# Performance work log

Hardware: AMD Instinct MI355X
Metric: run time of the kernel (lower is better)

## Reference

```python
import jax, jax.numpy as jnp
import numpy as np

B, N, S, DG, C_IN, C_OUT, HID = 2, 128, 4, 8, 4, 8, 32


def setup_inputs() -> dict:
    key = jax.random.key(0)
    ks = jax.random.split(key, 10)

    def w(k, shape, fan_in):
        return jax.random.normal(k, shape, jnp.float32) / np.float32(np.sqrt(fan_in))

    return {
        "pairwise_g": jax.random.normal(ks[0], (B, N, N, S, S, DG), jnp.float32),
        "coset_functions": jax.random.normal(ks[1], (B, N, S, C_IN), jnp.float32),
        "mask": jax.random.bernoulli(ks[2], 0.9, (B, N, S)),
        "ky_W1": w(ks[3], (C_IN, HID, 2), 2), "ky_b1": jnp.zeros((C_IN, HID), jnp.float32),
        "ky_W2": w(ks[4], (C_IN, HID, HID), HID), "ky_b2": jnp.zeros((C_IN, HID), jnp.float32),
        "ky_W3": w(ks[5], (C_IN, 1, HID), HID), "ky_b3": jnp.zeros((C_IN, 1), jnp.float32),
        "kg_W1": w(ks[6], (C_IN, HID, DG), DG), "kg_b1": jnp.zeros((C_IN, HID), jnp.float32),
        "kg_W2": w(ks[7], (C_IN, HID, HID), HID), "kg_b2": jnp.zeros((C_IN, HID), jnp.float32),
        "kg_W3": w(ks[8], (C_IN, 1, HID), HID), "kg_b3": jnp.zeros((C_IN, 1), jnp.float32),
        "w_out": w(ks[9], (C_OUT, C_IN), C_IN),
    }


def _mlp(x, W1, b1, W2, b2, W3, b3):
    # NerualNetKernel with bn=False, act=Swish: (Linear + SiLU) x 3, incl. output layer.
    h = jax.nn.silu(x @ W1.T + b1)
    h = jax.nn.silu(h @ W2.T + b2)
    return jax.nn.silu(h @ W3.T + b3)


def reference(pairwise_g, coset_functions, mask,
              ky_W1, ky_b1, ky_W2, ky_b2, ky_W3, ky_b3,
              kg_W1, kg_b1, kg_W2, kg_b2, kg_W3, kg_b3, w_out):
    b, n, _, s, _, _ = pairwise_g.shape
    c_in = coset_functions.shape[-1]
    key_mask = mask[:, None, :, None, :, None]  # (B,1,N,1,S,1) masks key points/samples
    outs = []
    for i in range(c_in):  # fixed small channel loop, as in the original module
        f = coset_functions[..., i:i + 1]  # (B,N,S,1)
        y1 = jnp.broadcast_to(f[:, None, :, None, :, :], (b, n, n, s, s, 1))  # key side
        y2 = jnp.broadcast_to(f[:, :, None, :, None, :], (b, n, n, s, s, 1))  # query side
        y = jnp.concatenate([y1, y2], axis=-1)  # (B,N,N,S,S,2)
        k = (_mlp(y, ky_W1[i], ky_b1[i], ky_W2[i], ky_b2[i], ky_W3[i], ky_b3[i])
             + _mlp(pairwise_g, kg_W1[i], kg_b1[i], kg_W2[i], kg_b2[i], kg_W3[i], kg_b3[i]))
        att = jnp.where(key_mask, jnp.exp(k), jnp.zeros((), k.dtype))  # (B,N,N,S,S,1)
        att = att / att.sum(axis=(2, 4), keepdims=True)
        f = f + (att * f[:, None, :, None, :, :]).sum(axis=(2, 4))  # residual + weighted agg
        outs.append(f)
    cf = jnp.concatenate(outs, axis=-1)  # (B,N,S,C_IN)
    cf = cf * mask[..., None].astype(cf.dtype)
    return cf @ w_out.T  # (B,N,S,C_OUT), bias-free output transform
```

## Files before the change

kernel.cpp:

```cpp
#include <hip/hip_runtime.h>
#include <hip/hip_bf16.h>

#define BB   2
#define NN   128
#define SS   4
#define DGG  8
#define CIN  4
#define COUT 8
#define HH   32
#define NT   512

typedef __attribute__((ext_vector_type(4))) float          fvec4;
typedef __attribute__((ext_vector_type(4))) unsigned short usvec4;
typedef __attribute__((ext_vector_type(8))) unsigned short usvec8;
typedef __attribute__((ext_vector_type(2))) __fp16         half2v;
typedef __attribute__((ext_vector_type(8))) __fp16         f16x8;
typedef __attribute__((ext_vector_type(4))) float          f32x4;
typedef __attribute__((ext_vector_type(4))) unsigned int   uvec4;

__device__ __forceinline__ float bf2f(unsigned short u) {
    return __uint_as_float(((unsigned int)u) << 16);
}
__device__ __forceinline__ float silu_f(float x) {
    float e = __builtin_amdgcn_exp2f(x * -1.44269504f);
    return x * __builtin_amdgcn_rcpf(1.0f + e);
}
__device__ __forceinline__ float exp_f(float x) {
    return __builtin_amdgcn_exp2f(x * 1.44269504f);
}

__device__ __forceinline__ unsigned int pk2u(float a, float b) {
#if __has_builtin(__builtin_amdgcn_cvt_pkrtz)
    half2v h = __builtin_amdgcn_cvt_pkrtz(a, b);
#else
    half2v h; h[0] = (__fp16)a; h[1] = (__fp16)b;
#endif
    union { half2v h; unsigned int u; } x; x.h = h; return x.u;
}
union FU { uvec4 u; f16x8 h; };
__device__ __forceinline__ f16x8 mk_frag(unsigned a, unsigned b, unsigned c, unsigned d) {
    FU x; x.u = (uvec4){a, b, c, d}; return x.h;
}
__device__ __forceinline__ f16x8 mk_fragv(uvec4 u) {
    FU x; x.u = u; return x.h;
}
__device__ __forceinline__ uvec4 vldu(const unsigned* p) {
    return *(volatile const uvec4*)p;
}
__device__ __forceinline__ fvec4 vldf(const float* p) {
    return *(volatile const fvec4*)p;
}
__device__ __forceinline__ f16x8 silu_frag(f32x4 a, f32x4 b) {
    return mk_frag(pk2u(silu_f(a[0]), silu_f(a[1])),
                   pk2u(silu_f(a[2]), silu_f(a[3])),
                   pk2u(silu_f(b[0]), silu_f(b[1])),
                   pk2u(silu_f(b[2]), silu_f(b[3])));
}

__device__ __forceinline__ float loadS(const void* p, int idx, int fmode) {
    return fmode ? bf2f(((const unsigned short*)p)[idx])
                 : ((const float*)p)[idx];
}
__device__ __forceinline__ void load8(const void* p, int base, int fmode, float* dst) {
    if (fmode) {
        usvec8 v = *(const usvec8*)((const unsigned short*)p + base);
#pragma unroll
        for (int d = 0; d < 8; ++d) dst[d] = bf2f(v[d]);
    } else {
        fvec4 a = *(const fvec4*)((const float*)p + base);
        fvec4 b = *(const fvec4*)((const float*)p + base + 4);
        dst[0] = a[0]; dst[1] = a[1]; dst[2] = a[2]; dst[3] = a[3];
        dst[4] = b[0]; dst[5] = b[1]; dst[6] = b[2]; dst[7] = b[3];
    }
}
__device__ __forceinline__ int load_mask(const void* p, int idx, int mmode) {
    if (mmode == 0) return ((const int*)p)[idx] != 0;
    if (mmode == 1) return ((const unsigned short*)p)[idx] != 0;
    if (mmode == 2) return ((const unsigned char*)p)[idx] != 0;
    return ((const unsigned int*)p)[idx] != 0;
}
__device__ __forceinline__ void stage_pk(unsigned int* dst, const void* src,
                                         int pairs, int fmode, int tid) {
    if (fmode) {
        const unsigned short* s = (const unsigned short*)src;
        for (int x = tid; x < pairs; x += NT)
            dst[x] = pk2u(bf2f(s[2 * x]), bf2f(s[2 * x + 1]));
    } else {
        const float* s = (const float*)src;
        for (int x = tid; x < pairs; x += NT)
            dst[x] = pk2u(s[2 * x], s[2 * x + 1]);
    }
}
__device__ __forceinline__ void copy_arr(float* sm, const void* src, int off,
                                         int cnt, int fmode, int tid) {
    if (fmode) {
        const unsigned short* s = (const unsigned short*)src;
        for (int x = tid; x < cnt; x += NT) sm[off + x] = bf2f(s[x]);
    } else {
        const float* s = (const float*)src;
        for (int x = tid; x < cnt; x += NT) sm[off + x] = s[x];
    }
}
__device__ __forceinline__ void detect_inline(const void* g_mask, const void* g_coset,
                                              int tid, int* smi, int slot) {
    if (tid < 64) {
        const unsigned short* cu = (const unsigned short*)g_coset;
        unsigned short v = cu[2 * tid];
        int e = (v >> 7) & 0xFF;
        int hits = __popcll(__ballot(e >= 110 && e <= 135));
        int fmode_ = (hits > 32) ? 1 : 0;
        const unsigned short* mu = (const unsigned short*)g_mask;
        int evenBF = 0, any3 = 0, anyByte = 0;
        for (int r = 0; r < 8; ++r) {
            int idx = tid + r * 64;
            unsigned short m = mu[idx];
            if (m == 0x3F80) { any3 = 1; if (!(idx & 1)) evenBF = 1; }
            if (m == 0x0101 || m == 0x0100) anyByte = 1;
        }
        evenBF  = (__ballot(evenBF)  != 0ull);
        any3    = (__ballot(any3)    != 0ull);
        anyByte = (__ballot(anyByte) != 0ull);
        if (tid == 0) {
            smi[slot]     = fmode_;
            smi[slot + 1] = evenBF ? 1 : (any3 ? 3 : (anyByte ? 2 : 0));
        }
    }
}

#define UG_G    0
#define F_FA    2048
#define U_YW1n  4096
#define U_GW1   4608
#define U_GB1q  5120
#define U_W2Y   5632
#define U_W2G   7680
#define F_YB2   9728
#define F_GB2   9856
#define U_YW3   9984
#define U_GW3   10048
#define F_YB3   10112
#define F_GB3   10116
#define U_CB1   10120
#define F_RED   10128
#define F_MODE  10192
#define U_TOTAL 10194

__global__ __launch_bounds__(NT, 8) void emha_mfma(
    const void* __restrict__ g_pw, const void* __restrict__ g_coset,
    const void* __restrict__ g_mask,
    const void* yW1, const void* yb1, const void* yW2, const void* yb2,
    const void* yW3, const void* yb3,
    const void* gW1, const void* gb1, const void* gW2, const void* gb2,
    const void* gW3, const void* gb3,
    const void* wout, void* outp)
{
    __shared__ __align__(16) unsigned int smu[U_TOTAL];
    float* smf = (float*)smu;
    int*   smi = (int*)smu;
    const int tid = threadIdx.x;

    detect_inline(g_mask, g_coset, tid, smi, F_MODE);
    __syncthreads();
    const int fmode = smi[F_MODE];
    const int mmode = smi[F_MODE + 1];
    __syncthreads();

    const int bn = blockIdx.x >> 2;
    const int s1 = blockIdx.x & 3;
    const int b  = bn >> 7;
    const int n1 = bn & 127;

    {
        const int pos = tid;
        const int n2 = pos >> 2, s2 = pos & 3;
        float g8[8];
        load8(g_pw, (((bn * NN + n2) * SS + s1) * SS + s2) * DGG, fmode, g8);
#pragma unroll
        for (int q = 0; q < 4; ++q)
            smu[UG_G + pos * 4 + q] = pk2u(g8[2 * q], g8[2 * q + 1]);
    }
    for (int x = tid; x < 2048; x += NT)
        smf[F_FA + x] = loadS(g_coset, b * 2048 + x, fmode);
    for (int x = tid; x < 128; x += NT) {
        smu[U_YW1n + x * 4 + 0] = pk2u(loadS(yW1, 2 * x, fmode), loadS(yW1, 2 * x + 1, fmode));
        smu[U_YW1n + x * 4 + 1] = pk2u(loadS(yb1, x, fmode), 0.f);
        smu[U_YW1n + x * 4 + 2] = 0u;
        smu[U_YW1n + x * 4 + 3] = 0u;
        smu[U_GB1q + x * 4 + 0] = pk2u(loadS(gb1, x, fmode), 0.f);
        smu[U_GB1q + x * 4 + 1] = 0u;
        smu[U_GB1q + x * 4 + 2] = 0u;
        smu[U_GB1q + x * 4 + 3] = 0u;
    }
    stage_pk(&smu[U_GW1], gW1, 512,  fmode, tid);
    stage_pk(&smu[U_W2Y], yW2, 2048, fmode, tid);
    stage_pk(&smu[U_W2G], gW2, 2048, fmode, tid);
    stage_pk(&smu[U_YW3], yW3, 64,   fmode, tid);
    stage_pk(&smu[U_GW3], gW3, 64,   fmode, tid);
    copy_arr(smf, yb2, F_YB2, 128, fmode, tid);
    copy_arr(smf, gb2, F_GB2, 128, fmode, tid);
    copy_arr(smf, yb3, F_YB3, 4, fmode, tid);
    copy_arr(smf, gb3, F_GB3, 4, fmode, tid);
    if (tid < 8) smu[U_CB1 + tid] = (tid == 0) ? 0x00003C00u : 0u;
    __syncthreads();

    const int lane = tid & 63;
    const int wave = tid >> 6;
    const int quad = lane >> 4;
    const int col  = lane & 15;
    const int qpos = n1 * 4 + s1;
    const int h0   = ((col >> 2) << 3) + (col & 3);

    const int mymask = load_mask(g_mask, b * 512 + wave * 64 + lane, mmode);
    const unsigned long long km64 = __ballot(mymask != 0);

    const unsigned* Zp = &smu[U_CB1 + 4];
    const f32x4 zf = {0.f, 0.f, 0.f, 0.f};

#pragma unroll 1
    for (int ci = 0; ci < CIN; ++ci) {
        const int rowy = (ci * 32 + h0) * 4;
        const unsigned* pAY1a = (quad == 0) ? &smu[U_YW1n + rowy] : Zp;
        const unsigned* pAY1b = (quad == 0) ? &smu[U_YW1n + rowy + 16] : Zp;
        const unsigned* pGA = (quad == 0) ? &smu[U_GW1 + rowy]
                            : ((quad == 1) ? &smu[U_GB1q + rowy] : Zp);
        const unsigned* pGB = (quad == 0) ? &smu[U_GW1 + rowy + 16]
                            : ((quad == 1) ? &smu[U_GB1q + rowy + 16] : Zp);
        const unsigned* pW2 = &smu[U_W2Y + ci * 512 + h0 * 16 + quad * 4];
        const float*    pCb = &smf[F_YB2 + ci * 32 + quad * 8];
        const unsigned* pA3y = (col == 0) ? &smu[U_YW3 + ci * 16 + quad * 4] : Zp;
        const unsigned* pA3g = (col == 0) ? &smu[U_GW3 + ci * 16 + quad * 4] : Zp;
        const unsigned* pBg = (quad == 0) ? &smu[UG_G + (wave * 64 + col) * 4]
                            : ((quad == 1) ? &smu[U_CB1] : Zp);
        const int stepBg = (quad == 0) ? 64 : 0;
        const float* pFA = &smf[F_FA + (wave * 64 + col) * 4 + ci];

        const float fb  = smf[F_FA + qpos * 4 + ci];
        const float b3y = smf[F_YB3 + ci];
        const float b3g = smf[F_GB3 + ci];

        float aN = 0.f, aD = 0.f;
        int amt = col;
#pragma unroll 1
        for (int t = 0; t < 4; ++t) {
            const uvec4 gq = vldu(pBg);
            const float fap = *(volatile const float*)pFA;
            const f16x8 Bg1 = mk_fragv(gq);
            const f16x8 B1y = mk_frag(pk2u(fap, fb), 0x00003C00u, 0u, 0u);

            f32x4 d1a, d1b, dga, dgb;
            {
                const f16x8 AY1a = mk_fragv(vldu(pAY1a));
                const f16x8 AY1b = mk_fragv(vldu(pAY1b));
                const f16x8 GA   = mk_fragv(vldu(pGA));
                const f16x8 GB   = mk_fragv(vldu(pGB));
#if defined(__HIP_DEVICE_COMPILE__)
                d1a = __builtin_amdgcn_mfma_f32_16x16x32_f16(AY1a, B1y, zf, 0, 0, 0);
                d1b = __builtin_amdgcn_mfma_f32_16x16x32_f16(AY1b, B1y, zf, 0, 0, 0);
                dga = __builtin_amdgcn_mfma_f32_16x16x32_f16(GA,   Bg1, zf, 0, 0, 0);
                dgb = __builtin_amdgcn_mfma_f32_16x16x32_f16(GB,   Bg1, zf, 0, 0, 0);
#else
                d1a = zf; d1b = zf; dga = zf; dgb = zf;
#endif
            }
            const f16x8 By = silu_frag(d1a, d1b);
            const f16x8 Bg = silu_frag(dga, dgb);

            f32x4 dy0, dy1, dg0, dg1;
            {
#if defined(__HIP_DEVICE_COMPILE__)
                dy0 = __builtin_amdgcn_mfma_f32_16x16x32_f16(mk_fragv(vldu(pW2)),        By, vldf(pCb),       0, 0, 0);
                dy1 = __builtin_amdgcn_mfma_f32_16x16x32_f16(mk_fragv(vldu(pW2 + 64)),   By, vldf(pCb + 4),   0, 0, 0);
                dg0 = __builtin_amdgcn_mfma_f32_16x16x32_f16(mk_fragv(vldu(pW2 + 2048)), Bg, vldf(pCb + 128), 0, 0, 0);
                dg1 = __builtin_amdgcn_mfma_f32_16x16x32_f16(mk_fragv(vldu(pW2 + 2112)), Bg, vldf(pCb + 132), 0, 0, 0);
#else
                dy0 = zf; dy1 = zf; dg0 = zf; dg1 = zf;
#endif
            }
            const f16x8 By2 = silu_frag(dy0, dy1);
            const f16x8 Bg2 = silu_frag(dg0, dg1);

            f32x4 dy3, dg3;
#if defined(__HIP_DEVICE_COMPILE__)
            dy3 = __builtin_amdgcn_mfma_f32_16x16x32_f16(mk_fragv(vldu(pA3y)), By2, zf, 0, 0, 0);
            dg3 = __builtin_amdgcn_mfma_f32_16x16x32_f16(mk_fragv(vldu(pA3g)), Bg2, zf, 0, 0, 0);
#else
            dy3 = zf; dg3 = zf;
#endif
            const float kyv = silu_f(dy3[0] + b3y);
            const float kgv = silu_f(dg3[0] + b3g);
            const int   kb  = (int)((km64 >> amt) & 1ull);
            const float e = kb ? exp_f(kyv + kgv) : 0.f;
            aD += e;
            aN += e * fap;

            amt += 16;
            pBg += stepBg;
            pFA += 64;
        }
        aN += __shfl_xor(aN, 1);  aD += __shfl_xor(aD, 1);
        aN += __shfl_xor(aN, 2);  aD += __shfl_xor(aD, 2);
        aN += __shfl_xor(aN, 4);  aD += __shfl_xor(aD, 4);
        aN += __shfl_xor(aN, 8);  aD += __shfl_xor(aD, 8);
        if (lane == 0) {
            smf[F_RED + (wave * 4 + ci) * 2 + 0] = aN;
            smf[F_RED + (wave * 4 + ci) * 2 + 1] = aD;
        }
    }
    __syncthreads();

    if (tid < COUT) {
        const int o = tid;
        const int m1 = load_mask(g_mask, b * 512 + qpos, mmode);
        float acc = 0.f;
#pragma unroll
        for (int ci = 0; ci < CIN; ++ci) {
            float N = 0.f, D = 0.f;
#pragma unroll
            for (int w = 0; w < 8; ++w) {
                N += smf[F_RED + (w * 4 + ci) * 2 + 0];
                D += smf[F_RED + (w * 4 + ci) * 2 + 1];
            }
            const float fbv = smf[F_FA + qpos * 4 + ci];
            const float cf = m1 ? (fbv + N / D) : 0.f;
            acc += cf * loadS(wout, o * CIN + ci, fmode);
        }
        const int oidx = (bn * SS + s1) * COUT + o;
        if (fmode) ((__hip_bfloat16*)outp)[oidx] = __float2bfloat16(acc);
        else       ((float*)outp)[oidx] = acc;
    }
}

extern "C" void kernel_launch(void* const* d_in, const int* in_sizes, int n_in,
                              void* d_out, int out_size, void* d_ws, size_t ws_size,
                              hipStream_t stream) {
    emha_mfma<<<BB * NN * SS, NT, 0, stream>>>(
        d_in[0], d_in[1], d_in[2],
        d_in[3], d_in[4], d_in[5], d_in[6], d_in[7], d_in[8],
        d_in[9], d_in[10], d_in[11], d_in[12], d_in[13], d_in[14],
        d_in[15], d_out);
}
```

Baseline: 197.7 us.

## Halve block size, hoist weight fragments into registers, drop volatile loads

Cuts threads per block from 512 to 256, so each wave now handles 128 key positions in 8 iterations instead of 64 in 4. The per-channel MLP weight and bias fragments are loaded from shared memory once, before the inner loop, rather than through volatile loads on every iteration. The mask ballot is split into two 64-bit masks, and the first barrier is merged so that mask loading overlaps staging. This trades more registers and fewer waves per block for less LDS traffic and more instruction-level parallelism.

New measurement: 168.9 us. 1.17x faster.

```diff
diff --git a/kernel.cpp b/kernel.cpp
--- a/kernel.cpp
+++ b/kernel.cpp
@@ -8,7 +8,7 @@
 #define CIN  4
 #define COUT 8
 #define HH   32
-#define NT   512
+#define NT   256
 
 typedef __attribute__((ext_vector_type(4))) float          fvec4;
 typedef __attribute__((ext_vector_type(4))) unsigned short usvec4;
@@ -43,12 +43,6 @@
 }
 __device__ __forceinline__ f16x8 mk_fragv(uvec4 u) {
     FU x; x.u = u; return x.h;
-}
-__device__ __forceinline__ uvec4 vldu(const unsigned* p) {
-    return *(volatile const uvec4*)p;
-}
-__device__ __forceinline__ fvec4 vldf(const float* p) {
-    return *(volatile const fvec4*)p;
 }
 __device__ __forceinline__ f16x8 silu_frag(f32x4 a, f32x4 b) {
     return mk_frag(pk2u(silu_f(a[0]), silu_f(a[1])),
@@ -142,10 +136,10 @@
 #define F_GB3   10116
 #define U_CB1   10120
 #define F_RED   10128
-#define F_MODE  10192
-#define U_TOTAL 10194
-
-__global__ __launch_bounds__(NT, 8) void emha_mfma(
+#define F_MODE  10160
+#define U_TOTAL 10162
+
+__global__ __launch_bounds__(NT, 4) void emha_mfma(
     const void* __restrict__ g_pw, const void* __restrict__ g_coset,
     const void* __restrict__ g_mask,
     const void* yW1, const void* yb1, const void* yW2, const void* yb2,
@@ -170,8 +164,9 @@
     const int b  = bn >> 7;
     const int n1 = bn & 127;
 
-    {
-        const int pos = tid;
+#pragma unroll
+    for (int it = 0; it < 2; ++it) {
+        const int pos = tid + it * 256;
         const int n2 = pos >> 2, s2 = pos & 3;
         float g8[8];
         load8(g_pw, (((bn * NN + n2) * SS + s1) * SS + s2) * DGG, fmode, g8);
@@ -201,99 +196,96 @@
     copy_arr(smf, yb3, F_YB3, 4, fmode, tid);
     copy_arr(smf, gb3, F_GB3, 4, fmode, tid);
     if (tid < 8) smu[U_CB1 + tid] = (tid == 0) ? 0x00003C00u : 0u;
-    __syncthreads();
 
     const int lane = tid & 63;
     const int wave = tid >> 6;
+    const int mLo = load_mask(g_mask, b * 512 + wave * 128 + lane, mmode);
+    const int mHi = load_mask(g_mask, b * 512 + wave * 128 + 64 + lane, mmode);
+    const unsigned long long kmL = __ballot(mLo != 0);
+    const unsigned long long kmH = __ballot(mHi != 0);
+    __syncthreads();
+
     const int quad = lane >> 4;
     const int col  = lane & 15;
     const int qpos = n1 * 4 + s1;
     const int h0   = ((col >> 2) << 3) + (col & 3);
-
-    const int mymask = load_mask(g_mask, b * 512 + wave * 64 + lane, mmode);
-    const unsigned long long km64 = __ballot(mymask != 0);
-
     const unsigned* Zp = &smu[U_CB1 + 4];
     const f32x4 zf = {0.f, 0.f, 0.f, 0.f};
 
 #pragma unroll 1
     for (int ci = 0; ci < CIN; ++ci) {
         const int rowy = (ci * 32 + h0) * 4;
-        const unsigned* pAY1a = (quad == 0) ? &smu[U_YW1n + rowy] : Zp;
-        const unsigned* pAY1b = (quad == 0) ? &smu[U_YW1n + rowy + 16] : Zp;
-        const unsigned* pGA = (quad == 0) ? &smu[U_GW1 + rowy]
-                            : ((quad == 1) ? &smu[U_GB1q + rowy] : Zp);
-        const unsigned* pGB = (quad == 0) ? &smu[U_GW1 + rowy + 16]
-                            : ((quad == 1) ? &smu[U_GB1q + rowy + 16] : Zp);
-        const unsigned* pW2 = &smu[U_W2Y + ci * 512 + h0 * 16 + quad * 4];
-        const float*    pCb = &smf[F_YB2 + ci * 32 + quad * 8];
-        const unsigned* pA3y = (col == 0) ? &smu[U_YW3 + ci * 16 + quad * 4] : Zp;
-        const unsigned* pA3g = (col == 0) ? &smu[U_GW3 + ci * 16 + quad * 4] : Zp;
-        const unsigned* pBg = (quad == 0) ? &smu[UG_G + (wave * 64 + col) * 4]
-                            : ((quad == 1) ? &smu[U_CB1] : Zp);
-        const int stepBg = (quad == 0) ? 64 : 0;
-        const float* pFA = &smf[F_FA + (wave * 64 + col) * 4 + ci];
+        const f16x8 AY1a = mk_fragv(*(const uvec4*)((quad == 0) ? &smu[U_YW1n + rowy] : Zp));
+        const f16x8 AY1b = mk_fragv(*(const uvec4*)((quad == 0) ? &smu[U_YW1n + rowy + 16] : Zp));
+        const f16x8 GA = mk_fragv(*(const uvec4*)((quad == 0) ? &smu[U_GW1 + rowy]
+                                   : (quad == 1) ? &smu[U_GB1q + rowy] : Zp));
+        const f16x8 GB = mk_fragv(*(const uvec4*)((quad == 0) ? &smu[U_GW1 + rowy + 16]
+                                   : (quad == 1) ? &smu[U_GB1q + rowy + 16] : Zp));
+        const f16x8 Ay0 = mk_fragv(*(const uvec4*)&smu[U_W2Y + ci * 512 + h0 * 16 + quad * 4]);
+        const f16x8 Ay1 = mk_fragv(*(const uvec4*)&smu[U_W2Y + ci * 512 + (h0 + 4) * 16 + quad * 4]);
+        const f16x8 Ag0 = mk_fragv(*(const uvec4*)&smu[U_W2G + ci * 512 + h0 * 16 + quad * 4]);
+        const f16x8 Ag1 = mk_fragv(*(const uvec4*)&smu[U_W2G + ci * 512 + (h0 + 4) * 16 + quad * 4]);
+        const fvec4 cY0 = *(const fvec4*)&smf[F_YB2 + ci * 32 + quad * 8];
+        const fvec4 cY1 = *(const fvec4*)&smf[F_YB2 + ci * 32 + quad * 8 + 4];
+        const fvec4 cG0 = *(const fvec4*)&smf[F_GB2 + ci * 32 + quad * 8];
+        const fvec4 cG1 = *(const fvec4*)&smf[F_GB2 + ci * 32 + quad * 8 + 4];
+        const f16x8 A3y = mk_fragv(*(const uvec4*)((col == 0) ? &smu[U_YW3 + ci * 16 + quad * 4] : Zp));
+        const f16x8 A3g = mk_fragv(*(const uvec4*)((col == 0) ? &smu[U_GW3 + ci * 16 + quad * 4] : Zp));
 
         const float fb  = smf[F_FA + qpos * 4 + ci];
         const float b3y = smf[F_YB3 + ci];
         const float b3g = smf[F_GB3 + ci];
 
+        const unsigned* pBg = (quad == 0) ? &smu[UG_G + (wave * 128 + col) * 4]
+                            : ((quad == 1) ? &smu[U_CB1] : Zp);
+        const int stepBg = (quad == 0) ? 64 : 0;
+        const float* pFA = &smf[F_FA + (wave * 128 + col) * 4 + ci];
+
         float aN = 0.f, aD = 0.f;
-        int amt = col;
-#pragma unroll 1
-        for (int t = 0; t < 4; ++t) {
-            const uvec4 gq = vldu(pBg);
-            const float fap = *(volatile const float*)pFA;
+#pragma unroll 2
+        for (int t = 0; t < 8; ++t) {
+            const uvec4 gq = *(const uvec4*)pBg;
+            const float fap = *pFA;
             const f16x8 Bg1 = mk_fragv(gq);
             const f16x8 B1y = mk_frag(pk2u(fap, fb), 0x00003C00u, 0u, 0u);
 
-            f32x4 d1a, d1b, dga, dgb;
-            {
-                const f16x8 AY1a = mk_fragv(vldu(pAY1a));
-                const f16x8 AY1b = mk_fragv(vldu(pAY1b));
-                const f16x8 GA   = mk_fragv(vldu(pGA));
-                const f16x8 GB   = mk_fragv(vldu(pGB));
+            f32x4 d1a, d1b, dga, dgb, dy0, dy1, dg0, dg1, dy3, dg3;
 #if defined(__HIP_DEVICE_COMPILE__)
-                d1a = __builtin_amdgcn_mfma_f32_16x16x32_f16(AY1a, B1y, zf, 0, 0, 0);
-                d1b = __builtin_amdgcn_mfma_f32_16x16x32_f16(AY1b, B1y, zf, 0, 0, 0);
-                dga = __builtin_amdgcn_mfma_f32_16x16x32_f16(GA,   Bg1, zf, 0, 0, 0);
-                dgb = __builtin_amdgcn_mfma_f32_16x16x32_f16(GB,   Bg1, zf, 0, 0, 0);
+            d1a = __builtin_amdgcn_mfma_f32_16x16x32_f16(AY1a, B1y, zf, 0, 0, 0);
+            d1b = __builtin_amdgcn_mfma_f32_16x16x32_f16(AY1b, B1y, zf, 0, 0, 0);
+            dga = __builtin_amdgcn_mfma_f32_16x16x32_f16(GA,   Bg1, zf, 0, 0, 0);
+            dgb = __builtin_amdgcn_mfma_f32_16x16x32_f16(GB,   Bg1, zf, 0, 0, 0);
 #else
-                d1a = zf; d1b = zf; dga = zf; dgb = zf;
+            d1a = zf; d1b = zf; dga = zf; dgb = zf;
 #endif
-            }
             const f16x8 By = silu_frag(d1a, d1b);
             const f16x8 Bg = silu_frag(dga, dgb);
 
-            f32x4 dy0, dy1, dg0, dg1;
-            {
 #if defined(__HIP_DEVICE_COMPILE__)
-                dy0 = __builtin_amdgcn_mfma_f32_16x16x32_f16(mk_fragv(vldu(pW2)),        By, vldf(pCb),       0, 0, 0);
-                dy1 = __builtin_amdgcn_mfma_f32_16x16x32_f16(mk_fragv(vldu(pW2 + 64)),   By, vldf(pCb + 4),   0, 0, 0);
-                dg0 = __builtin_amdgcn_mfma_f32_16x16x32_f16(mk_fragv(vldu(pW2 + 2048)), Bg, vldf(pCb + 128), 0, 0, 0);
-                dg1 = __builtin_amdgcn_mfma_f32_16x16x32_f16(mk_fragv(vldu(pW2 + 2112)), Bg, vldf(pCb + 132), 0, 0, 0);
+            dy0 = __builtin_amdgcn_mfma_f32_16x16x32_f16(Ay0, By, cY0, 0, 0, 0);
+            dy1 = __builtin_amdgcn_mfma_f32_16x16x32_f16(Ay1, By, cY1, 0, 0, 0);
+            dg0 = __builtin_amdgcn_mfma_f32_16x16x32_f16(Ag0, Bg, cG0, 0, 0, 0);
+            dg1 = __builtin_amdgcn_mfma_f32_16x16x32_f16(Ag1, Bg, cG1, 0, 0, 0);
 #else
-                dy0 = zf; dy1 = zf; dg0 = zf; dg1 = zf;
+            dy0 = cY0; dy1 = cY1; dg0 = cG0; dg1 = cG1;
 #endif
-            }
             const f16x8 By2 = silu_frag(dy0, dy1);
             const f16x8 Bg2 = silu_frag(dg0, dg1);
 
-            f32x4 dy3, dg3;
 #if defined(__HIP_DEVICE_COMPILE__)
-            dy3 = __builtin_amdgcn_mfma_f32_16x16x32_f16(mk_fragv(vldu(pA3y)), By2, zf, 0, 0, 0);
-            dg3 = __builtin_amdgcn_mfma_f32_16x16x32_f16(mk_fragv(vldu(pA3g)), Bg2, zf, 0, 0, 0);
+            dy3 = __builtin_amdgcn_mfma_f32_16x16x32_f16(A3y, By2, zf, 0, 0, 0);
+            dg3 = __builtin_amdgcn_mfma_f32_16x16x32_f16(A3g, Bg2, zf, 0, 0, 0);
 #else
             dy3 = zf; dg3 = zf;
 #endif
             const float kyv = silu_f(dy3[0] + b3y);
             const float kgv = silu_f(dg3[0] + b3g);
-            const int   kb  = (int)((km64 >> amt) & 1ull);
+            const unsigned long long sel = (t < 4) ? kmL : kmH;
+            const int kb = (int)((sel >> (((t & 3) << 4) + col)) & 1);
             const float e = kb ? exp_f(kyv + kgv) : 0.f;
             aD += e;
             aN += e * fap;
 
-            amt += 16;
             pBg += stepBg;
             pFA += 64;
         }
@@ -316,7 +308,7 @@
         for (int ci = 0; ci < CIN; ++ci) {
             float N = 0.f, D = 0.f;
 #pragma unroll
-            for (int w = 0; w < 8; ++w) {
+            for (int w = 0; w < 4; ++w) {
                 N += smf[F_RED + (w * 4 + ci) * 2 + 0];
                 D += smf[F_RED + (w * 4 + ci) * 2 + 1];
             }
```
